# Performance work log

Measured on AMD Instinct MI355X. Metric: run time of the kernel, lower is better.

## Reference

```python
import jax, jax.numpy as jnp
import numpy as np

NEG_SLOPE = 0.2
EPS = 1e-8

def add_self_loops(edge_index, n_nodes):
    loops = jnp.arange(n_nodes, dtype=edge_index.dtype)
    return jnp.concatenate([edge_index, jnp.stack([loops, loops])], axis=1)

def gatv2_layer(x, edge_index, Wl, Wr, att, bias, concat):
    # x: [N, Fin], edge_index: [2, E] (row0=src j, row1=dst i), att: [H, Fout]
    N = x.shape[0]
    H, Fo = att.shape
    ei = add_self_loops(edge_index, N)
    src, dst = ei[0], ei[1]
    xl = (x @ Wl).reshape(N, H, Fo)
    xr = (x @ Wr).reshape(N, H, Fo)
    s = xl[src] + xr[dst]                                   # [E, H, Fo]
    e = jnp.einsum('ehf,hf->eh', jax.nn.leaky_relu(s, NEG_SLOPE), att)  # [E, H]
    # segment softmax over edges sharing the same destination node
    m = jax.ops.segment_max(e, dst, num_segments=N)          # [N, H]
    ex = jnp.exp(e - m[dst])
    den = jax.ops.segment_sum(ex, dst, num_segments=N)
    alpha = ex / (den[dst] + 1e-16)                          # [E, H]
    out = jax.ops.segment_sum(xl[src] * alpha[:, :, None], dst, num_segments=N)  # [N, H, Fo]
    out = out.reshape(N, H * Fo) if concat else out.mean(axis=1)
    return out + bias

def forward_once(x, edge_index, W1l, W1r, att1, b1, W2l, W2r, att2, b2):
    # eval mode: dropouts are identity
    h = jax.nn.elu(gatv2_layer(x, edge_index, W1l, W1r, att1, b1, concat=True))
    return gatv2_layer(h, edge_index, W2l, W2r, att2, b2, concat=False)

def reference(x1, edge_index1, x2, edge_index2, W1l, W1r, att1, b1, W2l, W2r, att2, b2):
    y = forward_once(x1, edge_index1, W1l, W1r, att1, b1, W2l, W2r, att2, b2)
    z = forward_once(x2, edge_index2, W1l, W1r, att1, b1, W2l, W2r, att2, b2)
    logp_y = jax.nn.log_softmax(y, axis=1)
    logp_z = jax.nn.log_softmax(z, axis=1)
    ny = jnp.maximum(jnp.linalg.norm(y, axis=1), EPS)
    nz = jnp.maximum(jnp.linalg.norm(z, axis=1), EPS)
    cos = jnp.sum(y * z, axis=1) / (ny * nz)
    return (logp_y, 1.0 - cos, logp_z, logp_y, logp_y)

def setup_inputs() -> dict:
    key = jax.random.key(0)
    ks = jax.random.split(key, 12)
    N, E, Fin, HID, H, C = 50000, 800000, 256, 32, 8, 16
    g = lambda k, shape, fan: jax.random.normal(k, shape, jnp.float32) * (1.0 / np.sqrt(fan))
    return {
        'x1': jax.random.normal(ks[0], (N, Fin), jnp.float32),
        'edge_index1': jax.random.randint(ks[1], (2, E), 0, N, jnp.int32),
        'x2': jax.random.normal(ks[2], (N, Fin), jnp.float32),
        'edge_index2': jax.random.randint(ks[3], (2, E), 0, N, jnp.int32),
        'W1l': g(ks[4], (Fin, H * HID), Fin),
        'W1r': g(ks[5], (Fin, H * HID), Fin),
        'att1': g(ks[6], (H, HID), HID),
        'b1': jnp.zeros((H * HID,), jnp.float32),
        'W2l': g(ks[7], (H * HID, 1 * C), H * HID),
        'W2r': g(ks[8], (H * HID, 1 * C), H * HID),
        'att2': g(ks[9], (1, C), C),
        'b2': jnp.zeros((C,), jnp.float32),
    }
```

## Files before the change

### kernel.cpp

```cpp
#include <hip/hip_runtime.h>
#include <hip/hip_bf16.h>
#include <math.h>

#define FIN 256
#define F1  256
#define C2  16
#define NEG 0.2f

typedef short bf16x8 __attribute__((ext_vector_type(8)));
typedef float f32x4v __attribute__((ext_vector_type(4)));
typedef float f32x2 __attribute__((ext_vector_type(2)));

__device__ __forceinline__ float bf2f(unsigned short u) {
  union { float f; unsigned int i; } c; c.i = ((unsigned int)u) << 16; return c.f;
}
__device__ __forceinline__ unsigned short f2bf(float f) {
  __hip_bfloat16 b = __float2bfloat16(f);
  return *(unsigned short*)&b;
}
__device__ __forceinline__ f32x2 bfpair(unsigned int u) {
  union { float f; unsigned int i; } lo, hi;
  lo.i = u << 16;
  hi.i = u & 0xffff0000u;
  f32x2 r; r.x = lo.f; r.y = hi.f; return r;
}

__global__ __launch_bounds__(256) void deg_kernel(const int* __restrict__ dst,
                                                  int* __restrict__ deg, int E) {
  int e = blockIdx.x * blockDim.x + threadIdx.x;
  if (e < E) atomicAdd(&deg[dst[e]], 1);
}

__global__ __launch_bounds__(1024) void scan_part_kernel(const int* __restrict__ deg,
    int* __restrict__ offs, int* __restrict__ partials, int n) {
  __shared__ int wsum[16], wpref[16];
  int tid = threadIdx.x, lane = tid & 63, wid = tid >> 6;
  int idx = blockIdx.x * 1024 + tid;
  int v = (idx < n) ? deg[idx] : 0;
  int s = v;
#pragma unroll
  for (int o = 1; o < 64; o <<= 1) {
    int t = __shfl_up(s, o, 64);
    if (lane >= o) s += t;
  }
  if (lane == 63) wsum[wid] = s;
  __syncthreads();
  if (tid < 16) {
    int t = wsum[tid];
    int ss = t;
#pragma unroll
    for (int o = 1; o < 16; o <<= 1) {
      int u = __shfl_up(ss, o, 16);
      if (tid >= o) ss += u;
    }
    wpref[tid] = ss - t;
    if (tid == 15) partials[blockIdx.x] = ss;
  }
  __syncthreads();
  if (idx < n) offs[idx] = wpref[wid] + s - v;
}

__global__ __launch_bounds__(1024) void scan_fix_kernel(int* __restrict__ offs,
    const int* __restrict__ partials, int nb, int n) {
  __shared__ int carry_s;
  int tid = threadIdx.x;
  int b = blockIdx.x;
  if (tid < 64) {
    int v = (tid < nb) ? partials[tid] : 0;
    int s = v;
#pragma unroll
    for (int o = 1; o < 64; o <<= 1) {
      int t = __shfl_up(s, o, 64);
      if (tid >= o) s += t;
    }
    if (b == 0) {
      if (tid == nb - 1) offs[n] = s;
    } else if (tid == b - 1) {
      carry_s = s;
    }
  }
  __syncthreads();
  if (b > 0) {
    int idx = b * 1024 + tid;
    if (idx < n) offs[idx] += carry_s;
  }
}

__global__ __launch_bounds__(256) void fill_kernel(const int* __restrict__ src,
    const int* __restrict__ dst, const int* __restrict__ offs,
    int* __restrict__ cnt, int* __restrict__ csr, int E) {
  int e = blockIdx.x * blockDim.x + threadIdx.x;
  if (e < E) {
    int d = dst[e];
    int pos = offs[d] + atomicAdd(&cnt[d], 1);
    csr[pos] = src[e];
  }
}

__global__ __launch_bounds__(256) void cvt_w_kernel(const float* __restrict__ Wl,
    const float* __restrict__ Wr, unsigned short* __restrict__ Wt) {
  int n = blockIdx.x;
  int k = threadIdx.x;
  float v = (n < 256) ? Wl[k * 256 + n] : Wr[k * 256 + (n - 256)];
  Wt[n * 256 + k] = f2bf(v);
}

__global__ __launch_bounds__(256) void cvt_w2_kernel(const float* __restrict__ Wl,
    const float* __restrict__ Wr, unsigned short* __restrict__ Wt2) {
  int c = blockIdx.x;
  int k = threadIdx.x;
  float v = (c < 16) ? Wl[k * 16 + c] : Wr[k * 16 + (c - 16)];
  Wt2[c * 256 + k] = f2bf(v);
}

#define LDT 72
__global__ __launch_bounds__(512) void gemm_mfma_kernel(
    const float* __restrict__ A, const unsigned short* __restrict__ Bt,
    unsigned short* __restrict__ C, int M) {
  __shared__ __align__(16) unsigned short As[128 * LDT];
  __shared__ __align__(16) unsigned short Bs[128 * LDT];
  int tid = threadIdx.x;
  int G = gridDim.x;
  int q = G >> 3, r = G & 7;
  int b = blockIdx.x;
  int xcd = b & 7, pos = b >> 3;
  int swz = (xcd < r) ? xcd * (q + 1) + pos : r * (q + 1) + (xcd - r) * q + pos;
  int row0 = (swz >> 2) * 128;
  int col0 = (swz & 3) * 128;
  int wid = tid >> 6, lane = tid & 63;
  int wr = wid >> 2, wc = wid & 3;
  int r16 = lane & 15, kb = (lane >> 4) * 8;

  f32x4v acc[4][2];
#pragma unroll
  for (int m = 0; m < 4; m++)
#pragma unroll
    for (int n = 0; n < 2; n++)
#pragma unroll
      for (int qq = 0; qq < 4; qq++) acc[m][n][qq] = 0.f;

  for (int k0 = 0; k0 < 256; k0 += 64) {
#pragma unroll
    for (int it = 0; it < 2; it++) {
      int g = tid + it * 512;
      int rr = g >> 3;
      int ko = (g & 7) * 8;
      int gr = row0 + rr;
      float4 a0 = make_float4(0.f, 0.f, 0.f, 0.f);
      float4 a1 = make_float4(0.f, 0.f, 0.f, 0.f);
      if (gr < M) {
        a0 = *(const float4*)&A[(size_t)gr * 256 + k0 + ko];
        a1 = *(const float4*)&A[(size_t)gr * 256 + k0 + ko + 4];
      }
      ushort4 lo, hi;
      lo.x = f2bf(a0.x); lo.y = f2bf(a0.y); lo.z = f2bf(a0.z); lo.w = f2bf(a0.w);
      hi.x = f2bf(a1.x); hi.y = f2bf(a1.y); hi.z = f2bf(a1.z); hi.w = f2bf(a1.w);
      *(ushort4*)&As[rr * LDT + ko] = lo;
      *(ushort4*)&As[rr * LDT + ko + 4] = hi;
      int4 bv = *(const int4*)&Bt[(size_t)(col0 + rr) * 256 + k0 + ko];
      *(int4*)&Bs[rr * LDT + ko] = bv;
    }
    __syncthreads();
#pragma unroll
    for (int kk = 0; kk < 64; kk += 32) {
      bf16x8 af[4], bfr[2];
#pragma unroll
      for (int m = 0; m < 4; m++)
        af[m] = *(const bf16x8*)&As[(wr * 64 + m * 16 + r16) * LDT + kk + kb];
#pragma unroll
      for (int n = 0; n < 2; n++)
        bfr[n] = *(const bf16x8*)&Bs[(wc * 32 + n * 16 + r16) * LDT + kk + kb];
#pragma unroll
      for (int m = 0; m < 4; m++)
#pragma unroll
        for (int n = 0; n < 2; n++)
          acc[m][n] = __builtin_amdgcn_mfma_f32_16x16x32_bf16(af[m], bfr[n], acc[m][n], 0, 0, 0);
    }
    __syncthreads();
  }
  int rq = (lane >> 4) * 4;
#pragma unroll
  for (int m = 0; m < 4; m++) {
#pragma unroll
    for (int n = 0; n < 2; n++) {
#pragma unroll
      for (int qq = 0; qq < 4; qq++) {
        int gr = row0 + wr * 64 + m * 16 + rq + qq;
        if (gr < M) {
          int gc = col0 + wc * 32 + n * 16 + r16;
          C[(size_t)gr * 512 + gc] = f2bf(acc[m][n][qq]);
        }
      }
    }
  }
}

#define LDB2 264
__global__ __launch_bounds__(256) void gemm2_mfma_kernel(
    const unsigned short* __restrict__ A, const unsigned short* __restrict__ Bt,
    unsigned short* __restrict__ C, int M) {
  __shared__ __align__(16) unsigned short As[256 * LDT];
  __shared__ __align__(16) unsigned short Bs[32 * LDB2];
  int tid = threadIdx.x;
  int row0 = blockIdx.x * 256;
  int wid = tid >> 6, lane = tid & 63;
  int r16 = lane & 15, kb = (lane >> 4) * 8, rq = (lane >> 4) * 4;

#pragma unroll
  for (int it = 0; it < 4; it++) {
    int g = tid + it * 256;
    int rr = g >> 5;
    int ko = (g & 31) * 8;
    *(int4*)&Bs[rr * LDB2 + ko] = *(const int4*)&Bt[rr * 256 + ko];
  }

  f32x4v acc[4][2];
#pragma unroll
  for (int m = 0; m < 4; m++)
#pragma unroll
    for (int n = 0; n < 2; n++)
#pragma unroll
      for (int qq = 0; qq < 4; qq++) acc[m][n][qq] = 0.f;

  for (int k0 = 0; k0 < 256; k0 += 64) {
#pragma unroll
    for (int it = 0; it < 8; it++) {
      int g = tid + it * 256;
      int rr = g >> 3;
      int ko = (g & 7) * 8;
      int gr = row0 + rr;
      int4 av = make_int4(0, 0, 0, 0);
      if (gr < M) av = *(const int4*)&A[(size_t)gr * 256 + k0 + ko];
      *(int4*)&As[rr * LDT + ko] = av;
    }
    __syncthreads();
#pragma unroll
    for (int kk = 0; kk < 64; kk += 32) {
      bf16x8 af[4], bfr[2];
#pragma unroll
      for (int m = 0; m < 4; m++)
        af[m] = *(const bf16x8*)&As[(wid * 64 + m * 16 + r16) * LDT + kk + kb];
#pragma unroll
      for (int n = 0; n < 2; n++)
        bfr[n] = *(const bf16x8*)&Bs[(n * 16 + r16) * LDB2 + k0 + kk + kb];
#pragma unroll
      for (int m = 0; m < 4; m++)
#pragma unroll
        for (int n = 0; n < 2; n++)
          acc[m][n] = __builtin_amdgcn_mfma_f32_16x16x32_bf16(af[m], bfr[n], acc[m][n], 0, 0, 0);
    }
    __syncthreads();
  }
#pragma unroll
  for (int m = 0; m < 4; m++) {
#pragma unroll
    for (int n = 0; n < 2; n++) {
#pragma unroll
      for (int qq = 0; qq < 4; qq++) {
        int gr = row0 + wid * 64 + m * 16 + rq + qq;
        if (gr < M) C[(size_t)gr * 32 + n * 16 + r16] = f2bf(acc[m][n][qq]);
      }
    }
  }
}

__global__ __launch_bounds__(256) void gat1_kernel(const unsigned short* __restrict__ xlr,
    const float* __restrict__ att, const float* __restrict__ bias,
    const int* __restrict__ offs, const int* __restrict__ csr,
    unsigned short* __restrict__ h, int N) {
  int w = threadIdx.x >> 6, lane = threadIdx.x & 63;
  int i = blockIdx.x * 4 + w;
  if (i >= N) return;
  i = __builtin_amdgcn_readfirstlane(i);
  const uint2* rows = (const uint2*)xlr;
  const uint2* rowi = rows + (size_t)i * 128;
  uint2 ul = rowi[lane];
  uint2 ur = rowi[64 + lane];
  f32x2 xl01 = bfpair(ul.x), xl23 = bfpair(ul.y);
  f32x2 xr01 = bfpair(ur.x), xr23 = bfpair(ur.y);
  float4 a4 = ((const float4*)att)[lane];
  f32x2 a01; a01.x = a4.x; a01.y = a4.y;
  f32x2 a23; a23.x = a4.z; a23.y = a4.w;

  f32x2 t01 = xl01 + xr01, t23 = xl23 + xr23;
  f32x2 l01 = __builtin_elementwise_max(t01, t01 * NEG);
  f32x2 l23 = __builtin_elementwise_max(t23, t23 * NEG);
  f32x2 ps = l01 * a01 + l23 * a23;
  float p = ps.x + ps.y;
  p += __shfl_xor(p, 1, 8);
  p += __shfl_xor(p, 2, 8);
  p += __shfl_xor(p, 4, 8);
  float m = p, ssum = 1.f;
  f32x2 O01 = xl01, O23 = xl23;

  int e = offs[i], end = offs[i + 1];
  int rem = end - e;

  int ja0 = __builtin_amdgcn_readfirstlane(rem > 0 ? csr[e + 0] : i);
  int ja1 = __builtin_amdgcn_readfirstlane(rem > 1 ? csr[e + 1] : i);
  uint2 ua0 = rows[(size_t)ja0 * 128 + lane];
  uint2 ua1 = rows[(size_t)ja1 * 128 + lane];
  int jb0 = __builtin_amdgcn_readfirstlane(rem > 2 ? csr[e + 2] : i);
  int jb1 = __builtin_amdgcn_readfirstlane(rem > 3 ? csr[e + 3] : i);
  uint2 ub0 = rows[(size_t)jb0 * 128 + lane];
  uint2 ub1 = rows[(size_t)jb1 * 128 + lane];
  int jc0 = __builtin_amdgcn_readfirstlane(rem > 4 ? csr[e + 4] : i);
  int jc1 = __builtin_amdgcn_readfirstlane(rem > 5 ? csr[e + 5] : i);
  uint2 uc0 = rows[(size_t)jc0 * 128 + lane];
  uint2 uc1 = rows[(size_t)jc1 * 128 + lane];

  while (rem >= 2) {
    int jn0 = __builtin_amdgcn_readfirstlane(rem > 6 ? csr[e + 6] : i);
    int jn1 = __builtin_amdgcn_readfirstlane(rem > 7 ? csr[e + 7] : i);
    uint2 un0 = rows[(size_t)jn0 * 128 + lane];
    uint2 un1 = rows[(size_t)jn1 * 128 + lane];
    f32x2 x001 = bfpair(ua0.x), x023 = bfpair(ua0.y);
    f32x2 x101 = bfpair(ua1.x), x123 = bfpair(ua1.y);
    f32x2 q01 = x001 + xr01, q23 = x023 + xr23;
    f32x2 r01 = x101 + xr01, r23 = x123 + xr23;
    f32x2 g01 = __builtin_elementwise_max(q01, q01 * NEG);
    f32x2 g23 = __builtin_elementwise_max(q23, q23 * NEG);
    f32x2 k01 = __builtin_elementwise_max(r01, r01 * NEG);
    f32x2 k23 = __builtin_elementwise_max(r23, r23 * NEG);
    f32x2 s0v = g01 * a01 + g23 * a23;
    f32x2 s1v = k01 * a01 + k23 * a23;
    float p0 = s0v.x + s0v.y;
    float p1 = s1v.x + s1v.y;
    p0 += __shfl_xor(p0, 1, 8);
    p1 += __shfl_xor(p1, 1, 8);
    p0 += __shfl_xor(p0, 2, 8);
    p1 += __shfl_xor(p1, 2, 8);
    p0 += __shfl_xor(p0, 4, 8);
    p1 += __shfl_xor(p1, 4, 8);
    float mx = fmaxf(p0, p1);
    if (!__all(mx <= m + 8.f)) {
      float mn = fmaxf(m, mx);
      float sc = __expf(m - mn);
      O01 *= sc; O23 *= sc; ssum *= sc; m = mn;
    }
    float w0 = __expf(p0 - m), w1 = __expf(p1 - m);
    O01 += w0 * x001 + w1 * x101;
    O23 += w0 * x023 + w1 * x123;
    ssum += w0 + w1;
    ua0 = ub0; ua1 = ub1;
    ub0 = uc0; ub1 = uc1;
    uc0 = un0; uc1 = un1;
    e += 2; rem -= 2;
  }
  if (rem == 1) {
    f32x2 x001 = bfpair(ua0.x), x023 = bfpair(ua0.y);
    f32x2 q01 = x001 + xr01, q23 = x023 + xr23;
    f32x2 g01 = __builtin_elementwise_max(q01, q01 * NEG);
    f32x2 g23 = __builtin_elementwise_max(q23, q23 * NEG);
    f32x2 s0v = g01 * a01 + g23 * a23;
    float p0 = s0v.x + s0v.y;
    p0 += __shfl_xor(p0, 1, 8);
    p0 += __shfl_xor(p0, 2, 8);
    p0 += __shfl_xor(p0, 4, 8);
    if (!__all(p0 <= m + 8.f)) {
      float mn = fmaxf(m, p0);
      float sc = __expf(m - mn);
      O01 *= sc; O23 *= sc; ssum *= sc; m = mn;
    }
    float w0 = __expf(p0 - m);
    O01 += w0 * x001;
    O23 += w0 * x023;
    ssum += w0;
  }
  float inv = 1.f / (ssum + 1e-16f);
  float4 b4 = ((const float4*)bias)[lane];
  float h0 = O01.x * inv + b4.x;
  float h1 = O01.y * inv + b4.y;
  float h2 = O23.x * inv + b4.z;
  float h3 = O23.y * inv + b4.w;
  h0 = h0 > 0.f ? h0 : (__expf(h0) - 1.f);
  h1 = h1 > 0.f ? h1 : (__expf(h1) - 1.f);
  h2 = h2 > 0.f ? h2 : (__expf(h2) - 1.f);
  h3 = h3 > 0.f ? h3 : (__expf(h3) - 1.f);
  ushort4 o;
  o.x = f2bf(h0); o.y = f2bf(h1); o.z = f2bf(h2); o.w = f2bf(h3);
  ((ushort4*)(h + (size_t)i * 256))[lane] = o;
}

__global__ __launch_bounds__(256) void gat2_kernel(const unsigned short* __restrict__ xlr2,
    const float* __restrict__ att, const float* __restrict__ b2,
    const int* __restrict__ offs, const int* __restrict__ csr,
    float* __restrict__ yout, int N) {
  int grp = threadIdx.x >> 4, c = threadIdx.x & 15;
  int i = blockIdx.x * 16 + grp;
  if (i >= N) return;
  float xli = bf2f(xlr2[(size_t)i * 32 + c]);
  float xri = bf2f(xlr2[(size_t)i * 32 + 16 + c]);
  float a = att[c];
  float v = xli + xri; v = fmaxf(v, NEG * v);
  float p = v * a;
#pragma unroll
  for (int o = 8; o >= 1; o >>= 1) p += __shfl_xor(p, o, 16);
  float m = p, ssum = 1.0f, O = xli;

  int e = offs[i], end = offs[i + 1];
  int rem = end - e;

  int ja0 = rem > 0 ? csr[e + 0] : i;
  int ja1 = rem > 1 ? csr[e + 1] : i;
  float xa0 = bf2f(xlr2[(size_t)ja0 * 32 + c]);
  float xa1 = bf2f(xlr2[(size_t)ja1 * 32 + c]);
  int jb0 = rem > 2 ? csr[e + 2] : i;
  int jb1 = rem > 3 ? csr[e + 3] : i;
  float xb0 = bf2f(xlr2[(size_t)jb0 * 32 + c]);
  float xb1 = bf2f(xlr2[(size_t)jb1 * 32 + c]);
  int jc0 = rem > 4 ? csr[e + 4] : i;
  int jc1 = rem > 5 ? csr[e + 5] : i;
  float xc0 = bf2f(xlr2[(size_t)jc0 * 32 + c]);
  float xc1 = bf2f(xlr2[(size_t)jc1 * 32 + c]);

  while (rem >= 2) {
    int jn0 = rem > 6 ? csr[e + 6] : i;
    int jn1 = rem > 7 ? csr[e + 7] : i;
    float xn0 = bf2f(xlr2[(size_t)jn0 * 32 + c]);
    float xn1 = bf2f(xlr2[(size_t)jn1 * 32 + c]);
    float q0 = xa0 + xri; q0 = fmaxf(q0, NEG * q0);
    float q1 = xa1 + xri; q1 = fmaxf(q1, NEG * q1);
    float p0 = q0 * a, p1 = q1 * a;
#pragma unroll
    for (int o = 8; o >= 1; o >>= 1) {
      p0 += __shfl_xor(p0, o, 16);
      p1 += __shfl_xor(p1, o, 16);
    }
    float mx = fmaxf(p0, p1);
    if (!__all(mx <= m + 8.f)) {
      float mn = fmaxf(m, mx);
      float sc = __expf(m - mn);
      O *= sc; ssum *= sc; m = mn;
    }
    float w0 = __expf(p0 - m), w1 = __expf(p1 - m);
    O += w0 * xa0 + w1 * xa1;
    ssum += w0 + w1;
    xa0 = xb0; xa1 = xb1;
    xb0 = xc0; xb1 = xc1;
    xc0 = xn0; xc1 = xn1;
    e += 2; rem -= 2;
  }
  if (rem == 1) {
    float q0 = xa0 + xri; q0 = fmaxf(q0, NEG * q0);
    float p0 = q0 * a;
#pragma unroll
    for (int o = 8; o >= 1; o >>= 1) p0 += __shfl_xor(p0, o, 16);
    if (!__all(p0 <= m + 8.f)) {
      float mn = fmaxf(m, p0);
      float sc = __expf(m - mn);
      O *= sc; ssum *= sc; m = mn;
    }
    float w0 = __expf(p0 - m);
    O += w0 * xa0;
    ssum += w0;
  }
  yout[(size_t)i * C2 + c] = O / (ssum + 1e-16f) + b2[c];
}

__global__ __launch_bounds__(256) void finalize_kernel(const float* __restrict__ y,
    const float* __restrict__ z, float* __restrict__ out, int N) {
  int grp = threadIdx.x >> 4, c = threadIdx.x & 15;
  int i = blockIdx.x * 16 + grp;
  if (i >= N) return;
  float yv = y[(size_t)i * C2 + c];
  float zv = z[(size_t)i * C2 + c];
  float my = yv;
#pragma unroll
  for (int o = 8; o >= 1; o >>= 1) my = fmaxf(my, __shfl_xor(my, o, 16));
  float sy = __expf(yv - my);
#pragma unroll
  for (int o = 8; o >= 1; o >>= 1) sy += __shfl_xor(sy, o, 16);
  float lpy = yv - my - __logf(sy);
  float mz = zv;
#pragma unroll
  for (int o = 8; o >= 1; o >>= 1) mz = fmaxf(mz, __shfl_xor(mz, o, 16));
  float sz = __expf(zv - mz);
#pragma unroll
  for (int o = 8; o >= 1; o >>= 1) sz += __shfl_xor(sz, o, 16);
  float lpz = zv - mz - __logf(sz);
  float dot = yv * zv, ny2 = yv * yv, nz2 = zv * zv;
#pragma unroll
  for (int o = 8; o >= 1; o >>= 1) {
    dot += __shfl_xor(dot, o, 16);
    ny2 += __shfl_xor(ny2, o, 16);
    nz2 += __shfl_xor(nz2, o, 16);
  }
  float ny = fmaxf(sqrtf(ny2), 1e-8f);
  float nz = fmaxf(sqrtf(nz2), 1e-8f);
  float cosv = dot / (ny * nz);
  size_t o1 = (size_t)N * C2;
  size_t o2 = o1 + N;
  size_t o3 = o2 + (size_t)N * C2;
  size_t o4 = o3 + (size_t)N * C2;
  size_t idx = (size_t)i * C2 + c;
  out[idx] = lpy;
  if (c == 0) out[o1 + i] = 1.0f - cosv;
  out[o2 + idx] = lpz;
  out[o3 + idx] = lpy;
  out[o4 + idx] = lpy;
}

extern "C" void kernel_launch(void* const* d_in, const int* in_sizes, int n_in,
                              void* d_out, int out_size, void* d_ws, size_t ws_size,
                              hipStream_t stream) {
  const float* x1   = (const float*)d_in[0];
  const int*   ei1  = (const int*)d_in[1];
  const float* x2   = (const float*)d_in[2];
  const int*   ei2  = (const int*)d_in[3];
  const float* W1l  = (const float*)d_in[4];
  const float* W1r  = (const float*)d_in[5];
  const float* att1 = (const float*)d_in[6];
  const float* b1   = (const float*)d_in[7];
  const float* W2l  = (const float*)d_in[8];
  const float* W2r  = (const float*)d_in[9];
  const float* att2 = (const float*)d_in[10];
  const float* b2   = (const float*)d_in[11];
  const int N = in_sizes[0] / FIN;
  const int E = in_sizes[1] / 2;
  float* out = (float*)d_out;

  char* w = (char*)d_ws;
  size_t off = 0;
  auto carve = [&](size_t bytes) -> void* {
    void* p = w + off;
    off += (bytes + 255) & ~(size_t)255;
    return p;
  };
  unsigned short* xlr_b = (unsigned short*)carve((size_t)N * 512 * 2);
  unsigned short* h     = (unsigned short*)carve((size_t)N * 256 * 2);
  unsigned short* Wt    = (unsigned short*)carve(512 * 256 * 2);
  unsigned short* Wt2   = (unsigned short*)carve(32 * 256 * 2);
  unsigned short* xlr2b = (unsigned short*)carve((size_t)N * 32 * 2);
  float* yb   = (float*)carve((size_t)N * 16 * 4);
  float* zb   = (float*)carve((size_t)N * 16 * 4);
  int* deg2 = (int*)carve((size_t)2 * N * 4);
  int* cnt2 = (int*)carve((size_t)2 * N * 4);
  int* offs = (int*)carve((size_t)(N + 1) * 4);
  int* csr  = (int*)carve((size_t)E * 4);
  int* partials = (int*)carve(64 * 4);
  (void)ws_size; (void)n_in; (void)out_size;

  const size_t zero_bytes = (size_t)((char*)cnt2 - (char*)deg2) + (size_t)2 * N * 4;
  hipMemsetAsync(deg2, 0, zero_bytes, stream);

  const int NB = (N + 1023) / 1024;

  cvt_w_kernel<<<512, 256, 0, stream>>>(W1l, W1r, Wt);
  cvt_w2_kernel<<<32, 256, 0, stream>>>(W2l, W2r, Wt2);

  for (int g = 0; g < 2; g++) {
    const float* x  = g ? x2 : x1;
    const int*   ei = g ? ei2 : ei1;
    float* yout = g ? zb : yb;
    int* deg = deg2 + (size_t)g * N;
    int* cnt = cnt2 + (size_t)g * N;
    const int* srcp = ei;
    const int* dstp = ei + E;

    deg_kernel<<<(E + 255) / 256, 256, 0, stream>>>(dstp, deg, E);
    scan_part_kernel<<<NB, 1024, 0, stream>>>(deg, offs, partials, N);
    scan_fix_kernel<<<NB, 1024, 0, stream>>>(offs, partials, NB, N);
    fill_kernel<<<(E + 255) / 256, 256, 0, stream>>>(srcp, dstp, offs, cnt, csr, E);

    int RB = (N + 127) / 128;
    gemm_mfma_kernel<<<RB * 4, 512, 0, stream>>>(x, Wt, xlr_b, N);
    gat1_kernel<<<(N + 3) / 4, 256, 0, stream>>>(xlr_b, att1, b1, offs, csr, h, N);
    gemm2_mfma_kernel<<<(N + 255) / 256, 256, 0, stream>>>(h, Wt2, xlr2b, N);
    gat2_kernel<<<(N + 15) / 16, 256, 0, stream>>>(xlr2b, att2, b2, offs, csr, yout, N);
  }
  finalize_kernel<<<(N + 15) / 16, 256, 0, stream>>>(yb, zb, out, N);
}
```

Baseline: 470.0 us.

## Batch both graphs into a single pass over a combined 2N-node problem

Concatenates the two input graphs into one 2N-node graph so that every stage (degree count, scan, CSR fill, both GEMMs, both attention kernels) runs once instead of twice. This halves the launch count and doubles the work per launch to improve GPU fill. It also splits the interleaved xl/xr buffers into separate arrays, giving the gather in gat1 a 512-byte row stride instead of 1024. The first-layer output h is written in place over xr, which gat1 reads, and that is only safe because each wave reads its own row of xr before writing it. The scan-fix kernel is widened to handle up to 1024 partial sums.

```diff
diff --git a/kernel.cpp b/kernel.cpp
--- a/kernel.cpp
+++ b/kernel.cpp
@@ -3,7 +3,6 @@
 #include <math.h>
 
 #define FIN 256
-#define F1  256
 #define C2  16
 #define NEG 0.2f
 
@@ -25,10 +24,15 @@
   f32x2 r; r.x = lo.f; r.y = hi.f; return r;
 }
 
-__global__ __launch_bounds__(256) void deg_kernel(const int* __restrict__ dst,
-                                                  int* __restrict__ deg, int E) {
-  int e = blockIdx.x * blockDim.x + threadIdx.x;
-  if (e < E) atomicAdd(&deg[dst[e]], 1);
+__global__ __launch_bounds__(256) void deg_kernel(const int* __restrict__ d1,
+    const int* __restrict__ d2, int* __restrict__ deg, int E, int N) {
+  int e = blockIdx.x * 256 + threadIdx.x;
+  if (e < 2 * E) {
+    int g = e >= E;
+    int le = g ? e - E : e;
+    int d = g ? d2[le] : d1[le];
+    atomicAdd(&deg[g * N + d], 1);
+  }
 }
 
 __global__ __launch_bounds__(1024) void scan_part_kernel(const int* __restrict__ deg,
@@ -62,22 +66,35 @@
 
 __global__ __launch_bounds__(1024) void scan_fix_kernel(int* __restrict__ offs,
     const int* __restrict__ partials, int nb, int n) {
+  __shared__ int wsum[16], wpref[16];
   __shared__ int carry_s;
-  int tid = threadIdx.x;
+  int tid = threadIdx.x, lane = tid & 63, wid = tid >> 6;
+  int v = (tid < nb) ? partials[tid] : 0;
+  int s = v;
+#pragma unroll
+  for (int o = 1; o < 64; o <<= 1) {
+    int t = __shfl_up(s, o, 64);
+    if (lane >= o) s += t;
+  }
+  if (lane == 63) wsum[wid] = s;
+  __syncthreads();
+  if (tid < 16) {
+    int t = wsum[tid];
+    int ss = t;
+#pragma unroll
+    for (int o = 1; o < 16; o <<= 1) {
+      int u = __shfl_up(ss, o, 16);
+      if (tid >= o) ss += u;
+    }
+    wpref[tid] = ss - t;
+  }
+  __syncthreads();
+  s += wpref[wid];
   int b = blockIdx.x;
-  if (tid < 64) {
-    int v = (tid < nb) ? partials[tid] : 0;
-    int s = v;
-#pragma unroll
-    for (int o = 1; o < 64; o <<= 1) {
-      int t = __shfl_up(s, o, 64);
-      if (tid >= o) s += t;
-    }
-    if (b == 0) {
-      if (tid == nb - 1) offs[n] = s;
-    } else if (tid == b - 1) {
-      carry_s = s;
-    }
+  if (b == 0) {
+    if (tid == nb - 1) offs[n] = s;
+  } else if (tid == b - 1) {
+    carry_s = s;
   }
   __syncthreads();
   if (b > 0) {
@@ -86,14 +103,19 @@
   }
 }
 
-__global__ __launch_bounds__(256) void fill_kernel(const int* __restrict__ src,
-    const int* __restrict__ dst, const int* __restrict__ offs,
-    int* __restrict__ cnt, int* __restrict__ csr, int E) {
-  int e = blockIdx.x * blockDim.x + threadIdx.x;
-  if (e < E) {
-    int d = dst[e];
-    int pos = offs[d] + atomicAdd(&cnt[d], 1);
-    csr[pos] = src[e];
+__global__ __launch_bounds__(256) void fill_kernel(const int* __restrict__ ei1,
+    const int* __restrict__ ei2, const int* __restrict__ offs,
+    int* __restrict__ cnt, int* __restrict__ csr, int E, int N) {
+  int e = blockIdx.x * 256 + threadIdx.x;
+  if (e < 2 * E) {
+    int g = e >= E;
+    int le = g ? e - E : e;
+    const int* ei = g ? ei2 : ei1;
+    int sN = ei[le];
+    int d  = ei[le + E];
+    int node = g * N + d;
+    int pos = offs[node] + atomicAdd(&cnt[node], 1);
+    csr[pos] = g * N + sN;
   }
 }
 
@@ -115,8 +137,10 @@
 
 #define LDT 72
 __global__ __launch_bounds__(512) void gemm_mfma_kernel(
-    const float* __restrict__ A, const unsigned short* __restrict__ Bt,
-    unsigned short* __restrict__ C, int M) {
+    const float* __restrict__ X1, const float* __restrict__ X2,
+    const unsigned short* __restrict__ Bt,
+    unsigned short* __restrict__ xlb, unsigned short* __restrict__ xrb,
+    int M, int NN) {
   __shared__ __align__(16) unsigned short As[128 * LDT];
   __shared__ __align__(16) unsigned short Bs[128 * LDT];
   int tid = threadIdx.x;
@@ -149,8 +173,10 @@
       float4 a0 = make_float4(0.f, 0.f, 0.f, 0.f);
       float4 a1 = make_float4(0.f, 0.f, 0.f, 0.f);
       if (gr < M) {
-        a0 = *(const float4*)&A[(size_t)gr * 256 + k0 + ko];
-        a1 = *(const float4*)&A[(size_t)gr * 256 + k0 + ko + 4];
+        const float* src = (gr < NN) ? &X1[(size_t)gr * 256]
+                                     : &X2[(size_t)(gr - NN) * 256];
+        a0 = *(const float4*)&src[k0 + ko];
+        a1 = *(const float4*)&src[k0 + ko + 4];
       }
       ushort4 lo, hi;
       lo.x = f2bf(a0.x); lo.y = f2bf(a0.y); lo.z = f2bf(a0.z); lo.w = f2bf(a0.w);
@@ -178,6 +204,8 @@
     }
     __syncthreads();
   }
+  unsigned short* Cb = (col0 < 256) ? xlb : xrb;
+  int cbase = (col0 & 255) + wc * 32;
   int rq = (lane >> 4) * 4;
 #pragma unroll
   for (int m = 0; m < 4; m++) {
@@ -187,8 +215,7 @@
       for (int qq = 0; qq < 4; qq++) {
         int gr = row0 + wr * 64 + m * 16 + rq + qq;
         if (gr < M) {
-          int gc = col0 + wc * 32 + n * 16 + r16;
-          C[(size_t)gr * 512 + gc] = f2bf(acc[m][n][qq]);
+          Cb[(size_t)gr * 256 + cbase + n * 16 + r16] = f2bf(acc[m][n][qq]);
         }
       }
     }
@@ -198,7 +225,7 @@
 #define LDB2 264
 __global__ __launch_bounds__(256) void gemm2_mfma_kernel(
     const unsigned short* __restrict__ A, const unsigned short* __restrict__ Bt,
-    unsigned short* __restrict__ C, int M) {
+    unsigned short* __restrict__ xl2b, unsigned short* __restrict__ xr2b, int M) {
   __shared__ __align__(16) unsigned short As[256 * LDT];
   __shared__ __align__(16) unsigned short Bs[32 * LDB2];
   int tid = threadIdx.x;
@@ -254,28 +281,26 @@
 #pragma unroll
   for (int m = 0; m < 4; m++) {
 #pragma unroll
-    for (int n = 0; n < 2; n++) {
-#pragma unroll
-      for (int qq = 0; qq < 4; qq++) {
-        int gr = row0 + wid * 64 + m * 16 + rq + qq;
-        if (gr < M) C[(size_t)gr * 32 + n * 16 + r16] = f2bf(acc[m][n][qq]);
+    for (int qq = 0; qq < 4; qq++) {
+      int gr = row0 + wid * 64 + m * 16 + rq + qq;
+      if (gr < M) {
+        xl2b[(size_t)gr * 16 + r16] = f2bf(acc[m][0][qq]);
+        xr2b[(size_t)gr * 16 + r16] = f2bf(acc[m][1][qq]);
       }
     }
   }
 }
 
-__global__ __launch_bounds__(256) void gat1_kernel(const unsigned short* __restrict__ xlr,
-    const float* __restrict__ att, const float* __restrict__ bias,
-    const int* __restrict__ offs, const int* __restrict__ csr,
-    unsigned short* __restrict__ h, int N) {
+__global__ __launch_bounds__(256) void gat1_kernel(const unsigned short* __restrict__ xlb,
+    unsigned short* xrb, const float* __restrict__ att, const float* __restrict__ bias,
+    const int* __restrict__ offs, const int* __restrict__ csr, int M) {
   int w = threadIdx.x >> 6, lane = threadIdx.x & 63;
   int i = blockIdx.x * 4 + w;
-  if (i >= N) return;
+  if (i >= M) return;
   i = __builtin_amdgcn_readfirstlane(i);
-  const uint2* rows = (const uint2*)xlr;
-  const uint2* rowi = rows + (size_t)i * 128;
-  uint2 ul = rowi[lane];
-  uint2 ur = rowi[64 + lane];
+  const uint2* rows = (const uint2*)xlb;
+  uint2 ul = rows[(size_t)i * 64 + lane];
+  uint2 ur = ((const uint2*)(xrb + (size_t)i * 256))[lane];
   f32x2 xl01 = bfpair(ul.x), xl23 = bfpair(ul.y);
   f32x2 xr01 = bfpair(ur.x), xr23 = bfpair(ur.y);
   float4 a4 = ((const float4*)att)[lane];
@@ -298,22 +323,22 @@
 
   int ja0 = __builtin_amdgcn_readfirstlane(rem > 0 ? csr[e + 0] : i);
   int ja1 = __builtin_amdgcn_readfirstlane(rem > 1 ? csr[e + 1] : i);
-  uint2 ua0 = rows[(size_t)ja0 * 128 + lane];
-  uint2 ua1 = rows[(size_t)ja1 * 128 + lane];
+  uint2 ua0 = rows[(size_t)ja0 * 64 + lane];
+  uint2 ua1 = rows[(size_t)ja1 * 64 + lane];
   int jb0 = __builtin_amdgcn_readfirstlane(rem > 2 ? csr[e + 2] : i);
   int jb1 = __builtin_amdgcn_readfirstlane(rem > 3 ? csr[e + 3] : i);
-  uint2 ub0 = rows[(size_t)jb0 * 128 + lane];
-  uint2 ub1 = rows[(size_t)jb1 * 128 + lane];
+  uint2 ub0 = rows[(size_t)jb0 * 64 + lane];
+  uint2 ub1 = rows[(size_t)jb1 * 64 + lane];
   int jc0 = __builtin_amdgcn_readfirstlane(rem > 4 ? csr[e + 4] : i);
   int jc1 = __builtin_amdgcn_readfirstlane(rem > 5 ? csr[e + 5] : i);
-  uint2 uc0 = rows[(size_t)jc0 * 128 + lane];
-  uint2 uc1 = rows[(size_t)jc1 * 128 + lane];
+  uint2 uc0 = rows[(size_t)jc0 * 64 + lane];
+  uint2 uc1 = rows[(size_t)jc1 * 64 + lane];
 
   while (rem >= 2) {
     int jn0 = __builtin_amdgcn_readfirstlane(rem > 6 ? csr[e + 6] : i);
     int jn1 = __builtin_amdgcn_readfirstlane(rem > 7 ? csr[e + 7] : i);
-    uint2 un0 = rows[(size_t)jn0 * 128 + lane];
-    uint2 un1 = rows[(size_t)jn1 * 128 + lane];
+    uint2 un0 = rows[(size_t)jn0 * 64 + lane];
+    uint2 un1 = rows[(size_t)jn1 * 64 + lane];
     f32x2 x001 = bfpair(ua0.x), x023 = bfpair(ua0.y);
     f32x2 x101 = bfpair(ua1.x), x123 = bfpair(ua1.y);
     f32x2 q01 = x001 + xr01, q23 = x023 + xr23;
@@ -379,18 +404,18 @@
   h3 = h3 > 0.f ? h3 : (__expf(h3) - 1.f);
   ushort4 o;
   o.x = f2bf(h0); o.y = f2bf(h1); o.z = f2bf(h2); o.w = f2bf(h3);
-  ((ushort4*)(h + (size_t)i * 256))[lane] = o;
-}
-
-__global__ __launch_bounds__(256) void gat2_kernel(const unsigned short* __restrict__ xlr2,
-    const float* __restrict__ att, const float* __restrict__ b2,
-    const int* __restrict__ offs, const int* __restrict__ csr,
-    float* __restrict__ yout, int N) {
+  ((ushort4*)(xrb + (size_t)i * 256))[lane] = o;
+}
+
+__global__ __launch_bounds__(256) void gat2_kernel(const unsigned short* __restrict__ xl2b,
+    const unsigned short* __restrict__ xr2b, const float* __restrict__ att,
+    const float* __restrict__ b2, const int* __restrict__ offs,
+    const int* __restrict__ csr, float* __restrict__ y2, int M) {
   int grp = threadIdx.x >> 4, c = threadIdx.x & 15;
   int i = blockIdx.x * 16 + grp;
-  if (i >= N) return;
-  float xli = bf2f(xlr2[(size_t)i * 32 + c]);
-  float xri = bf2f(xlr2[(size_t)i * 32 + 16 + c]);
+  if (i >= M) return;
+  float xli = bf2f(xl2b[(size_t)i * 16 + c]);
+  float xri = bf2f(xr2b[(size_t)i * 16 + c]);
   float a = att[c];
   float v = xli + xri; v = fmaxf(v, NEG * v);
   float p = v * a;
@@ -403,22 +428,22 @@
 
   int ja0 = rem > 0 ? csr[e + 0] : i;
   int ja1 = rem > 1 ? csr[e + 1] : i;
-  float xa0 = bf2f(xlr2[(size_t)ja0 * 32 + c]);
-  float xa1 = bf2f(xlr2[(size_t)ja1 * 32 + c]);
+  float xa0 = bf2f(xl2b[(size_t)ja0 * 16 + c]);
+  float xa1 = bf2f(xl2b[(size_t)ja1 * 16 + c]);
   int jb0 = rem > 2 ? csr[e + 2] : i;
   int jb1 = rem > 3 ? csr[e + 3] : i;
-  float xb0 = bf2f(xlr2[(size_t)jb0 * 32 + c]);
-  float xb1 = bf2f(xlr2[(size_t)jb1 * 32 + c]);
+  float xb0 = bf2f(xl2b[(size_t)jb0 * 16 + c]);
+  float xb1 = bf2f(xl2b[(size_t)jb1 * 16 + c]);
   int jc0 = rem > 4 ? csr[e + 4] : i;
   int jc1 = rem > 5 ? csr[e + 5] : i;
-  float xc0 = bf2f(xlr2[(size_t)jc0 * 32 + c]);
-  float xc1 = bf2f(xlr2[(size_t)jc1 * 32 + c]);
+  float xc0 = bf2f(xl2b[(size_t)jc0 * 16 + c]);
+  float xc1 = bf2f(xl2b[(size_t)jc1 * 16 + c]);
 
   while (rem >= 2) {
     int jn0 = rem > 6 ? csr[e + 6] : i;
     int jn1 = rem > 7 ? csr[e + 7] : i;
-    float xn0 = bf2f(xlr2[(size_t)jn0 * 32 + c]);
-    float xn1 = bf2f(xlr2[(size_t)jn1 * 32 + c]);
+    float xn0 = bf2f(xl2b[(size_t)jn0 * 16 + c]);
+    float xn1 = bf2f(xl2b[(size_t)jn1 * 16 + c]);
     float q0 = xa0 + xri; q0 = fmaxf(q0, NEG * q0);
     float q1 = xa1 + xri; q1 = fmaxf(q1, NEG * q1);
     float p0 = q0 * a, p1 = q1 * a;
@@ -455,7 +480,7 @@
     O += w0 * xa0;
     ssum += w0;
   }
-  yout[(size_t)i * C2 + c] = O / (ssum + 1e-16f) + b2[c];
+  y2[(size_t)i * C2 + c] = O / (ssum + 1e-16f) + b2[c];
 }
 
 __global__ __launch_bounds__(256) void finalize_kernel(const float* __restrict__ y,
@@ -518,6 +543,7 @@
   const float* b2   = (const float*)d_in[11];
   const int N = in_sizes[0] / FIN;
   const int E = in_sizes[1] / 2;
+  const int M = 2 * N;
   float* out = (float*)d_out;
 
   char* w = (char*)d_ws;
@@ -527,47 +553,38 @@
     off += (bytes + 255) & ~(size_t)255;
     return p;
   };
-  unsigned short* xlr_b = (unsigned short*)carve((size_t)N * 512 * 2);
-  unsigned short* h     = (unsigned short*)carve((size_t)N * 256 * 2);
-  unsigned short* Wt    = (unsigned short*)carve(512 * 256 * 2);
-  unsigned short* Wt2   = (unsigned short*)carve(32 * 256 * 2);
-  unsigned short* xlr2b = (unsigned short*)carve((size_t)N * 32 * 2);
-  float* yb   = (float*)carve((size_t)N * 16 * 4);
-  float* zb   = (float*)carve((size_t)N * 16 * 4);
-  int* deg2 = (int*)carve((size_t)2 * N * 4);
-  int* cnt2 = (int*)carve((size_t)2 * N * 4);
-  int* offs = (int*)carve((size_t)(N + 1) * 4);
-  int* csr  = (int*)carve((size_t)E * 4);
-  int* partials = (int*)carve(64 * 4);
+  unsigned short* xlb  = (unsigned short*)carve((size_t)M * 256 * 2);
+  unsigned short* xrb  = (unsigned short*)carve((size_t)M * 256 * 2);
+  unsigned short* Wt   = (unsigned short*)carve(512 * 256 * 2);
+  unsigned short* Wt2  = (unsigned short*)carve(32 * 256 * 2);
+  unsigned short* xl2b = (unsigned short*)carve((size_t)M * 16 * 2);
+  unsigned short* xr2b = (unsigned short*)carve((size_t)M * 16 * 2);
+  float* y2  = (float*)carve((size_t)M * 16 * 4);
+  int* deg  = (int*)carve((size_t)M * 4);
+  int* cnt  = (int*)carve((size_t)M * 4);
+  int* offs = (int*)carve((size_t)(M + 1) * 4);
+  int* csr  = (int*)carve((size_t)2 * E * 4);
+  int* partials = (int*)carve(128 * 4);
   (void)ws_size; (void)n_in; (void)out_size;
 
-  const size_t zero_bytes = (size_t)((char*)cnt2 - (char*)deg2) + (size_t)2 * N * 4;
-  hipMemsetAsync(deg2, 0, zero_bytes, stream);
-
-  const int NB = (N + 1023) / 1024;
+  const size_t zero_bytes = (size_t)((char*)cnt - (char*)deg) + (size_t)M * 4;
+  hipMemsetAsync(deg, 0, zero_bytes, stream);
+
+  const int NB = (M + 1023) / 1024;
 
   cvt_w_kernel<<<512, 256, 0, stream>>>(W1l, W1r, Wt);
   cvt_w2_kernel<<<32, 256, 0, stream>>>(W2l, W2r, Wt2);
 
-  for (int g = 0; g < 2; g++) {
-    const float* x  = g ? x2 : x1;
-    const int*   ei = g ? ei2 : ei1;
-    float* yout = g ? zb : yb;
-    int* deg = deg2 + (size_t)g * N;
-    int* cnt = cnt2 + (size_t)g * N;
-    const int* srcp = ei;
-    const int* dstp = ei + E;
-
-    deg_kernel<<<(E + 255) / 256, 256, 0, stream>>>(dstp, deg, E);
-    scan_part_kernel<<<NB, 1024, 0, stream>>>(deg, offs, partials, N);
-    scan_fix_kernel<<<NB, 1024, 0, stream>>>(offs, partials, NB, N);
-    fill_kernel<<<(E + 255) / 256, 256, 0, stream>>>(srcp, dstp, offs, cnt, csr, E);
-
-    int RB = (N + 127) / 128;
-    gemm_mfma_kernel<<<RB * 4, 512, 0, stream>>>(x, Wt, xlr_b, N);
-    gat1_kernel<<<(N + 3) / 4, 256, 0, stream>>>(xlr_b, att1, b1, offs, csr, h, N);
-    gemm2_mfma_kernel<<<(N + 255) / 256, 256, 0, stream>>>(h, Wt2, xlr2b, N);
-    gat2_kernel<<<(N + 15) / 16, 256, 0, stream>>>(xlr2b, att2, b2, offs, csr, yout, N);
-  }
-  finalize_kernel<<<(N + 15) / 16, 256, 0, stream>>>(yb, zb, out, N);
-}
+  deg_kernel<<<(2 * E + 255) / 256, 256, 0, stream>>>(ei1 + E, ei2 + E, deg, E, N);
+  scan_part_kernel<<<NB, 1024, 0, stream>>>(deg, offs, partials, M);
+  scan_fix_kernel<<<NB, 1024, 0, stream>>>(offs, partials, NB, M);
+  fill_kernel<<<(2 * E + 255) / 256, 256, 0, stream>>>(ei1, ei2, offs, cnt, csr, E, N);
+
+  int RB = (M + 127) / 128;
+  gemm_mfma_kernel<<<RB * 4, 512, 0, stream>>>(x1, x2, Wt, xlb, xrb, M, N);
+  gat1_kernel<<<(M + 3) / 4, 256, 0, stream>>>(xlb, xrb, att1, b1, offs, csr, M);
+  gemm2_mfma_kernel<<<(M + 255) / 256, 256, 0, stream>>>(xrb, Wt2, xl2b, xr2b, M);
+  gat2_kernel<<<(M + 15) / 16, 256, 0, stream>>>(xl2b, xr2b, att2, b2, offs, csr, y2, M);
+
+  finalize_kernel<<<(N + 15) / 16, 256, 0, stream>>>(y2, y2 + (size_t)N * 16, out, N);
+}
```

Measured after the change: 408.8 us. -13.0%, faster.
